# Performance work log

Hardware: AMD Instinct MI355X
Metric: run time of the kernel (lower is better)

The kernel has to match this reference:

```python
import jax, jax.numpy as jnp
import numpy as np

B, L, D, K = 1024, 50, 128, 20
NI, NL, NT = 100000, 10000, 2000  # items, locs, times


def _emb(k, n, d):
    e = jax.random.normal(k, (n, d), dtype=jnp.float32) * 0.02
    return e.at[0].set(0.0)  # padding_idx=0


def setup_inputs() -> dict:
    key = jax.random.key(0)
    ks = jax.random.split(key, 40)
    inp = {}
    inp['item'] = jax.random.randint(ks[0], (B, L), 0, NI)
    inp['locs'] = jax.random.randint(ks[1], (B,), 0, NL)
    inp['times'] = jax.random.randint(ks[2], (B,), 0, NT)
    inp['session_emb'] = jax.random.normal(ks[3], (B, 1, D), dtype=jnp.float32)
    # embedding tables
    inp['loc_emb'] = _emb(ks[4], NL, D)
    inp['time_emb'] = _emb(ks[5], NT, D)
    inp['item_emb'] = _emb(ks[6], NI, D)
    # sampled fixed-fanout neighbor tables Hg[edge]['neighbor']
    inp['nb_IL'] = jax.random.randint(ks[7], (NL, K), 0, NI)   # item neighbors of locs
    inp['nb_TL'] = jax.random.randint(ks[8], (NL, K), 0, NT)   # time neighbors of locs
    inp['nb_IT'] = jax.random.randint(ks[9], (NT, K), 0, NI)   # item neighbors of times
    inp['nb_LT'] = jax.random.randint(ks[10], (NT, K), 0, NL)  # loc neighbors of times
    inp['nb_II'] = jax.random.randint(ks[11], (NI, K), 0, NI)  # item neighbors of items
    inp['nb_LI'] = jax.random.randint(ks[12], (NI, K), 0, NL)  # loc neighbors of items
    inp['nb_TI'] = jax.random.randint(ks[13], (NI, K), 0, NT)  # time neighbors of items
    # 7 HeteAggregator params: Linear(2D -> D) + ReLU
    s = 1.0 / np.sqrt(2 * D)
    names = ['IL', 'TL', 'IT', 'LT', 'II', 'LI', 'TI']
    for i, nm in enumerate(names):
        inp['W_' + nm] = jax.random.uniform(ks[14 + i], (2 * D, D), jnp.float32, -s, s)
        inp['b_' + nm] = jnp.zeros((D,), jnp.float32)
    # 3 SemanticAttention params: Linear(D->D,bias)+tanh, Linear(D->1,no bias)
    s2 = 1.0 / np.sqrt(D)
    for i, nm in enumerate(['l', 't', 'i']):
        inp['Ws_' + nm] = jax.random.uniform(ks[24 + 3 * i], (D, D), jnp.float32, -s2, s2)
        inp['bs_' + nm] = jnp.zeros((D,), jnp.float32)
        inp['q_' + nm] = jax.random.uniform(ks[25 + 3 * i], (D, 1), jnp.float32, -s2, s2)
    return inp


def hete_agg(h_self, h_neigh, W, b):
    # h_self: [N, D]; h_neigh: [N, K, D] -> mean-aggregate, concat, linear, relu
    agg = h_neigh.mean(axis=1)
    return jax.nn.relu(jnp.concatenate([h_self, agg], axis=-1) @ W + b)


def sem_att(z, Ws, bs, q):
    # HAN-style semantic attention. z: [N, M, D]
    w = jnp.tanh(z @ Ws + bs) @ q          # [N, M, 1]
    beta = jax.nn.softmax(w.mean(axis=0), axis=0)  # [M, 1]
    return (beta[None] * z).sum(axis=1)    # [N, D]


def reference(item, locs, times, session_emb,
              loc_emb, time_emb, item_emb,
              nb_IL, nb_TL, nb_IT, nb_LT, nb_II, nb_LI, nb_TI,
              W_IL, b_IL, W_TL, b_TL, W_IT, b_IT, W_LT, b_LT,
              W_II, b_II, W_LI, b_LI, W_TI, b_TI,
              Ws_l, bs_l, q_l, Ws_t, bs_t, q_t, Ws_i, bs_i, q_i):
    iids = item.reshape(-1)  # [B*L]
    h_l_IL = hete_agg(loc_emb[locs], item_emb[nb_IL[locs]], W_IL, b_IL)
    h_l_TL = hete_agg(loc_emb[locs], time_emb[nb_TL[locs]], W_TL, b_TL)
    h_t_IT = hete_agg(time_emb[times], item_emb[nb_IT[times]], W_IT, b_IT)
    h_t_LT = hete_agg(time_emb[times], loc_emb[nb_LT[times]], W_LT, b_LT)
    h_i_II = hete_agg(item_emb[iids], item_emb[nb_II[iids]], W_II, b_II)
    h_i_LI = hete_agg(item_emb[iids], loc_emb[nb_LI[iids]], W_LI, b_LI)
    h_i_TI = hete_agg(item_emb[iids], time_emb[nb_TI[iids]], W_TI, b_TI)
    h_s = session_emb.squeeze(1)  # [B, D]
    h_l_stack = jnp.stack([h_l_IL, h_l_TL, h_s], axis=1)
    h_t_stack = jnp.stack([h_t_IT, h_t_LT, h_s], axis=1)
    h_i_stack = jnp.stack([h_i_II, h_i_TI, h_i_LI], axis=1)
    h_items = sem_att(h_i_stack, Ws_i, bs_i, q_i)
    h_locs = sem_att(h_l_stack, Ws_l, bs_l, q_l)
    h_times = sem_att(h_t_stack, Ws_t, bs_t, q_t)
    return (h_items, h_locs, h_times)
```

## Files before the change

kernel.cpp:

```cpp
#include <hip/hip_runtime.h>
#include <hip/hip_fp16.h>

#define DD 128
#define KK 20
#define TRR 32
#define NT 512

typedef unsigned int uint_t;
typedef unsigned short ushort_t;
typedef unsigned char uchar_t;
typedef _Float16 f16x8 __attribute__((ext_vector_type(8)));
typedef _Float16 f16x2 __attribute__((ext_vector_type(2)));
typedef float f32x4 __attribute__((ext_vector_type(4)));
typedef float f32x2 __attribute__((ext_vector_type(2)));

union UH { __half h; ushort_t s; };
union UF { f16x2 v[4]; uint4 u4; };

#if __has_builtin(__builtin_amdgcn_cvt_scalef32_pk_f16_fp8)
#define HAVE_SCALEF32 1
#endif

__device__ __forceinline__ float fast_tanh(float x) {
  const float e = __expf(2.f * x);
  return 1.f - 2.f / (e + 1.f);
}

__device__ __forceinline__ void f8acc(f16x2* a, const uint2 v) {
#ifdef HAVE_SCALEF32
  a[0] += __builtin_amdgcn_cvt_scalef32_pk_f16_fp8(v.x, 1.0f, false);
  a[1] += __builtin_amdgcn_cvt_scalef32_pk_f16_fp8(v.x, 1.0f, true);
  a[2] += __builtin_amdgcn_cvt_scalef32_pk_f16_fp8(v.y, 1.0f, false);
  a[3] += __builtin_amdgcn_cvt_scalef32_pk_f16_fp8(v.y, 1.0f, true);
#else
  f32x2 p;
  p = __builtin_amdgcn_cvt_pk_f32_fp8(v.x, false);
  a[0] += __builtin_amdgcn_cvt_pkrtz(p[0], p[1]);
  p = __builtin_amdgcn_cvt_pk_f32_fp8(v.x, true);
  a[1] += __builtin_amdgcn_cvt_pkrtz(p[0], p[1]);
  p = __builtin_amdgcn_cvt_pk_f32_fp8(v.y, false);
  a[2] += __builtin_amdgcn_cvt_pkrtz(p[0], p[1]);
  p = __builtin_amdgcn_cvt_pk_f32_fp8(v.y, true);
  a[3] += __builtin_amdgcn_cvt_pkrtz(p[0], p[1]);
#endif
}

struct CvtArgs {
  const float* item; const float* loc; const float* timet;
  ushort_t* dst16; uchar_t* dst8;
};

__global__ __launch_bounds__(256)
void k_cvt3(CvtArgs a) {
  const int t = blockIdx.x * blockDim.x + threadIdx.x;
  const float* src;
  if (t < 1600000) src = a.item + (size_t)t * 8;
  else if (t < 1760000) src = a.loc + ((size_t)t - 1600000) * 8;
  else src = a.timet + ((size_t)t - 1760000) * 8;
  const float4* ip = reinterpret_cast<const float4*>(src);
  const float4 x = ip[0], y = ip[1];
  UH h[8];
  h[0].h = __float2half_rn(x.x); h[1].h = __float2half_rn(x.y);
  h[2].h = __float2half_rn(x.z); h[3].h = __float2half_rn(x.w);
  h[4].h = __float2half_rn(y.x); h[5].h = __float2half_rn(y.y);
  h[6].h = __float2half_rn(y.z); h[7].h = __float2half_rn(y.w);
  uint4 o;
  o.x = (uint_t)h[0].s | ((uint_t)h[1].s << 16);
  o.y = (uint_t)h[2].s | ((uint_t)h[3].s << 16);
  o.z = (uint_t)h[4].s | ((uint_t)h[5].s << 16);
  o.w = (uint_t)h[6].s | ((uint_t)h[7].s << 16);
  reinterpret_cast<uint4*>(a.dst16)[t] = o;
  uint_t p0 = __builtin_amdgcn_cvt_pk_fp8_f32(x.x, x.y, 0u, false);
  p0 = __builtin_amdgcn_cvt_pk_fp8_f32(x.z, x.w, p0, true);
  uint_t p1 = __builtin_amdgcn_cvt_pk_fp8_f32(y.x, y.y, 0u, false);
  p1 = __builtin_amdgcn_cvt_pk_fp8_f32(y.z, y.w, p1, true);
  uint2 q; q.x = p0; q.y = p1;
  reinterpret_cast<uint2*>(a.dst8)[t] = q;
}

struct PackArgs {
  const float* src[10];
  ushort_t* dst;
};

__global__ __launch_bounds__(256)
void k_pack10(PackArgs a) {
  const int b = blockIdx.x, tid = threadIdx.x;
  int job, tin;
  size_t doff;
  if (b < 112) {
    job = b >> 4; tin = ((b & 15) << 8) | tid;
    doff = (size_t)job * 32768;
  } else {
    job = 7 + ((b - 112) >> 3); tin = (((b - 112) & 7) << 8) | tid;
    doff = 7ull * 32768 + (size_t)(job - 7) * 16384;
  }
  const float* W = a.src[job];
  const int l = tin & 63;
  const int ktnt = tin >> 6;
  const int nt = ktnt & 7;
  const int kt = ktnt >> 3;
  const int col = nt * 16 + (l & 15);
  const int kb = kt * 32 + ((l >> 4) << 3);
  UH h[8];
#pragma unroll
  for (int j = 0; j < 8; ++j) h[j].h = __float2half_rn(W[(size_t)(kb + j) * DD + col]);
  uint4 o;
  o.x = (uint_t)h[0].s | ((uint_t)h[1].s << 16);
  o.y = (uint_t)h[2].s | ((uint_t)h[3].s << 16);
  o.z = (uint_t)h[4].s | ((uint_t)h[5].s << 16);
  o.w = (uint_t)h[6].s | ((uint_t)h[7].s << 16);
  *reinterpret_cast<uint4*>(a.dst + doff + (size_t)ktnt * 512 + l * 8) = o;
}

struct MegaArgs {
  const int* item_idx; const ushort_t* item_t;
  const int* nbI[3]; const uchar_t* embI[3]; const ushort_t* pWI[3]; const float* bI[3];
  const ushort_t* pWsI; const float* bsI; const float* qI;
  ushort_t* hI; float* wsumI;
  const int* sidx[2]; const ushort_t* st[2];
  const int* nbS[2][2]; const uchar_t* embS[2][2];
  const ushort_t* pWS[2][2]; const float* bS[2][2];
  const ushort_t* pWsS[2]; const float* bsS[2]; const float* qS[2];
  const float* session;
  ushort_t* hS[2]; float* wsumS[2];
};

__global__ __launch_bounds__(NT, 6)
void k_mega(MegaArgs a) {
  __shared__ int ids[TRR];
  __shared__ int nidx[3][TRR][KK];
  __shared__ __align__(16) ushort_t xs[TRR][4 * DD + 8];
  __shared__ float red[8][TRR];

  const int tid = threadIdx.x;
  const int l = tid & 63;
  const int w = tid >> 6;
  const int bid = blockIdx.x;

  const bool isS = bid < 64;
  const int g = isS ? (bid >> 5) : 0;
  const int bl = isS ? (bid & 31) : (bid - 64);
  const int n0 = bl * TRR;

  const int* sidx;
  const ushort_t* selft;
  const int* nb_[3];
  const uchar_t* emb_[3];
  const ushort_t* pW_[3];
  const float* bias_[3];
  const ushort_t* pws; const float* bss; const float* qp;
  ushort_t* hd; float* wbase;
  if (!isS) {
    sidx = a.item_idx; selft = a.item_t;
    nb_[0] = a.nbI[0]; nb_[1] = a.nbI[1]; nb_[2] = a.nbI[2];
    emb_[0] = a.embI[0]; emb_[1] = a.embI[1]; emb_[2] = a.embI[2];
    pW_[0] = a.pWI[0]; pW_[1] = a.pWI[1]; pW_[2] = a.pWI[2];
    bias_[0] = a.bI[0]; bias_[1] = a.bI[1]; bias_[2] = a.bI[2];
    pws = a.pWsI; bss = a.bsI; qp = a.qI;
    hd = a.hI; wbase = a.wsumI;
  } else if (g == 0) {
    sidx = a.sidx[0]; selft = a.st[0];
    nb_[0] = a.nbS[0][0]; nb_[1] = a.nbS[0][1]; nb_[2] = nullptr;
    emb_[0] = a.embS[0][0]; emb_[1] = a.embS[0][1]; emb_[2] = nullptr;
    pW_[0] = a.pWS[0][0]; pW_[1] = a.pWS[0][1]; pW_[2] = nullptr;
    bias_[0] = a.bS[0][0]; bias_[1] = a.bS[0][1]; bias_[2] = nullptr;
    pws = a.pWsS[0]; bss = a.bsS[0]; qp = a.qS[0];
    hd = a.hS[0]; wbase = a.wsumS[0];
  } else {
    sidx = a.sidx[1]; selft = a.st[1];
    nb_[0] = a.nbS[1][0]; nb_[1] = a.nbS[1][1]; nb_[2] = nullptr;
    emb_[0] = a.embS[1][0]; emb_[1] = a.embS[1][1]; emb_[2] = nullptr;
    pW_[0] = a.pWS[1][0]; pW_[1] = a.pWS[1][1]; pW_[2] = nullptr;
    bias_[0] = a.bS[1][0]; bias_[1] = a.bS[1][1]; bias_[2] = nullptr;
    pws = a.pWsS[1]; bss = a.bsS[1]; qp = a.qS[1];
    hd = a.hS[1]; wbase = a.wsumS[1];
  }

  if (tid < TRR) ids[tid] = sidx[n0 + tid];
  __syncthreads();

  const int gr = tid >> 4;
  const int gsl = tid & 15;

#pragma unroll
  for (int e = 0; e < 3; ++e) {
    if (nb_[e]) {
      for (int t = tid; t < TRR * KK; t += NT) {
        const int rr = t / KK, kk = t - rr * KK;
        nidx[e][rr][kk] = nb_[e][(size_t)ids[rr] * KK + kk];
      }
    }
  }
  *reinterpret_cast<uint4*>(&xs[gr][gsl * 8]) =
      *reinterpret_cast<const uint4*>(selft + ((size_t)ids[gr] << 7) + gsl * 8);
  __syncthreads();

  const _Float16 sch = (_Float16)(1.f / KK);
  const f16x2 scv = (f16x2){sch, sch};
  if (!isS) {
    UF A0, A1, A2;
#pragma unroll
    for (int i = 0; i < 4; ++i) {
      A0.v[i] = (f16x2)0; A1.v[i] = (f16x2)0; A2.v[i] = (f16x2)0;
    }
#pragma unroll
    for (int kb = 0; kb < KK; kb += 4) {
      uint2 u0[4], u1[4], u2[4];
#pragma unroll
      for (int j = 0; j < 4; ++j)
        u0[j] = *reinterpret_cast<const uint2*>(emb_[0] + ((size_t)nidx[0][gr][kb + j] << 7) + gsl * 8);
#pragma unroll
      for (int j = 0; j < 4; ++j)
        u1[j] = *reinterpret_cast<const uint2*>(emb_[1] + ((size_t)nidx[1][gr][kb + j] << 7) + gsl * 8);
#pragma unroll
      for (int j = 0; j < 4; ++j)
        u2[j] = *reinterpret_cast<const uint2*>(emb_[2] + ((size_t)nidx[2][gr][kb + j] << 7) + gsl * 8);
#pragma unroll
      for (int j = 0; j < 4; ++j) {
        f8acc(A0.v, u0[j]); f8acc(A1.v, u1[j]); f8acc(A2.v, u2[j]);
      }
    }
#pragma unroll
    for (int i = 0; i < 4; ++i) {
      A0.v[i] *= scv; A1.v[i] *= scv; A2.v[i] *= scv;
    }
    *reinterpret_cast<uint4*>(&xs[gr][1 * DD + gsl * 8]) = A0.u4;
    *reinterpret_cast<uint4*>(&xs[gr][2 * DD + gsl * 8]) = A1.u4;
    *reinterpret_cast<uint4*>(&xs[gr][3 * DD + gsl * 8]) = A2.u4;
  } else {
    UF A0, A1;
#pragma unroll
    for (int i = 0; i < 4; ++i) { A0.v[i] = (f16x2)0; A1.v[i] = (f16x2)0; }
#pragma unroll
    for (int kb = 0; kb < KK; kb += 5) {
      uint2 u0[5], u1[5];
#pragma unroll
      for (int j = 0; j < 5; ++j)
        u0[j] = *reinterpret_cast<const uint2*>(emb_[0] + ((size_t)nidx[0][gr][kb + j] << 7) + gsl * 8);
#pragma unroll
      for (int j = 0; j < 5; ++j)
        u1[j] = *reinterpret_cast<const uint2*>(emb_[1] + ((size_t)nidx[1][gr][kb + j] << 7) + gsl * 8);
#pragma unroll
      for (int j = 0; j < 5; ++j) { f8acc(A0.v, u0[j]); f8acc(A1.v, u1[j]); }
    }
#pragma unroll
    for (int i = 0; i < 4; ++i) { A0.v[i] *= scv; A1.v[i] *= scv; }
    *reinterpret_cast<uint4*>(&xs[gr][1 * DD + gsl * 8]) = A0.u4;
    *reinterpret_cast<uint4*>(&xs[gr][2 * DD + gsl * 8]) = A1.u4;
    const float* srow = a.session + (size_t)(n0 + gr) * DD + gsl * 8;
    const float4 v0 = *reinterpret_cast<const float4*>(srow);
    const float4 v1 = *reinterpret_cast<const float4*>(srow + 4);
    UH h0, h1, h2, h3, h4, h5, h6, h7;
    h0.h = __float2half_rn(v0.x); h1.h = __float2half_rn(v0.y);
    h2.h = __float2half_rn(v0.z); h3.h = __float2half_rn(v0.w);
    h4.h = __float2half_rn(v1.x); h5.h = __float2half_rn(v1.y);
    h6.h = __float2half_rn(v1.z); h7.h = __float2half_rn(v1.w);
    uint4 o;
    o.x = (uint_t)h0.s | ((uint_t)h1.s << 16);
    o.y = (uint_t)h2.s | ((uint_t)h3.s << 16);
    o.z = (uint_t)h4.s | ((uint_t)h5.s << 16);
    o.w = (uint_t)h6.s | ((uint_t)h7.s << 16);
    *reinterpret_cast<uint4*>(&xs[gr][3 * DD + gsl * 8]) = o;
    *reinterpret_cast<uint4*>(hd + (size_t)(n0 + gr) * 3 * DD + 2 * DD + gsl * 8) = o;
  }
  __syncthreads();

  const int lcol = l & 15;
  const int g8 = (l >> 4) << 3;
  const int col0 = w * 16 + lcol;

#pragma unroll
  for (int e = 0; e < 3; ++e) {
    const bool full = (!isS) || (e < 2);
    if (full) {
      const ushort_t* pWp = pW_[e];
      const float* bp = bias_[e];
      f32x4 acc0, acc1;
      {
        const float b0 = bp[col0];
        acc0 = (f32x4){b0, b0, b0, b0};
        acc1 = acc0;
#pragma unroll
        for (int kt = 0; kt < 8; ++kt) {
          const int xcol = (kt < 4) ? (kt * 32 + g8) : (e * DD + kt * 32 + g8);
          const f16x8 Aa = *reinterpret_cast<const f16x8*>((const void*)&xs[lcol][xcol]);
          const f16x8 Ab = *reinterpret_cast<const f16x8*>((const void*)&xs[16 + lcol][xcol]);
          const f16x8 B = *reinterpret_cast<const f16x8*>(
              (const void*)(pWp + ((size_t)(kt * 8 + w) * 512) + l * 8));
          acc0 = __builtin_amdgcn_mfma_f32_16x16x32_f16(Aa, B, acc0, 0, 0, 0);
          acc1 = __builtin_amdgcn_mfma_f32_16x16x32_f16(Ab, B, acc1, 0, 0, 0);
        }
#pragma unroll
        for (int j = 0; j < 4; ++j) {
          acc0[j] = fmaxf(acc0[j], 0.f);
          acc1[j] = fmaxf(acc1[j], 0.f);
        }
      }
      __syncthreads();
      {
        const int rbase = (l >> 4) << 2;
#pragma unroll
        for (int j = 0; j < 4; ++j) {
          const int r0 = rbase + j, r1 = 16 + rbase + j;
          UH h0, h1;
          h0.h = __float2half_rn(acc0[j]);
          h1.h = __float2half_rn(acc1[j]);
          hd[(size_t)(n0 + r0) * 3 * DD + e * DD + col0] = h0.s;
          hd[(size_t)(n0 + r1) * 3 * DD + e * DD + col0] = h1.s;
          xs[r0][(e + 1) * DD + col0] = h0.s;
          xs[r1][(e + 1) * DD + col0] = h1.s;
        }
      }
      __syncthreads();
    }
    {
      const float b0 = bss[col0];
      f32x4 s0 = (f32x4){b0, b0, b0, b0};
      f32x4 s1 = s0;
#pragma unroll
      for (int kt = 0; kt < 4; ++kt) {
        const f16x8 Aa = *reinterpret_cast<const f16x8*>(
            (const void*)&xs[lcol][(e + 1) * DD + kt * 32 + g8]);
        const f16x8 Ab = *reinterpret_cast<const f16x8*>(
            (const void*)&xs[16 + lcol][(e + 1) * DD + kt * 32 + g8]);
        const f16x8 B = *reinterpret_cast<const f16x8*>(
            (const void*)(pws + ((size_t)(kt * 8 + w) * 512) + l * 8));
        s0 = __builtin_amdgcn_mfma_f32_16x16x32_f16(Aa, B, s0, 0, 0, 0);
        s1 = __builtin_amdgcn_mfma_f32_16x16x32_f16(Ab, B, s1, 0, 0, 0);
      }
      const float q0 = qp[col0];
      float p0[4], p1[4];
#pragma unroll
      for (int j = 0; j < 4; ++j) {
        p0[j] = fast_tanh(s0[j]) * q0;
        p1[j] = fast_tanh(s1[j]) * q0;
      }
#pragma unroll
      for (int off = 1; off < 16; off <<= 1) {
#pragma unroll
        for (int j = 0; j < 4; ++j) {
          p0[j] += __shfl_xor(p0[j], off, 64);
          p1[j] += __shfl_xor(p1[j], off, 64);
        }
      }
      if (lcol == 0) {
        const int rbase = (l >> 4) << 2;
#pragma unroll
        for (int j = 0; j < 4; ++j) {
          red[w][rbase + j] = p0[j];
          red[w][16 + rbase + j] = p1[j];
        }
      }
    }
    __syncthreads();
    if (tid < TRR) {
      float s = 0.f;
#pragma unroll
      for (int ww = 0; ww < 8; ++ww) s += red[ww][tid];
#pragma unroll
      for (int off = 1; off < 32; off <<= 1) s += __shfl_xor(s, off, 64);
      if (tid == 0) atomicAdd(&wbase[(bl & 63) * 4 + e], s);
    }
    __syncthreads();
  }
}

__global__ void k_beta(const float* __restrict__ wsum, float* __restrict__ beta) {
  if (threadIdx.x == 0 && blockIdx.x == 0) {
    const float invN[3] = {1.f / 51200.f, 1.f / 1024.f, 1.f / 1024.f};
    for (int g = 0; g < 3; ++g) {
      float s0 = 0.f, s1 = 0.f, s2 = 0.f;
      for (int bkt = 0; bkt < 64; ++bkt) {
        s0 += wsum[g * 256 + bkt * 4 + 0];
        s1 += wsum[g * 256 + bkt * 4 + 1];
        s2 += wsum[g * 256 + bkt * 4 + 2];
      }
      s0 *= invN[g]; s1 *= invN[g]; s2 *= invN[g];
      const float mx = fmaxf(s0, fmaxf(s1, s2));
      const float e0 = expf(s0 - mx), e1 = expf(s1 - mx), e2 = expf(s2 - mx);
      const float inv = 1.f / (e0 + e1 + e2);
      beta[g * 4 + 0] = e0 * inv;
      beta[g * 4 + 1] = e1 * inv;
      beta[g * 4 + 2] = e2 * inv;
    }
  }
}

__global__ void k_out(const ushort_t* __restrict__ h, const float* __restrict__ beta,
                      float* __restrict__ out) {
  const int idx = blockIdx.x * blockDim.x + threadIdx.x;
  const int row = idx >> 7;
  const int g = (row < 51200) ? 0 : ((row < 52224) ? 1 : 2);
  const float* bt = beta + g * 4;
  const size_t base = (size_t)idx + (size_t)row * 2 * DD;
  UH a, b, c;
  a.s = h[base]; b.s = h[base + DD]; c.s = h[base + 2 * DD];
  out[idx] = bt[0] * __half2float(a.h) + bt[1] * __half2float(b.h) +
             bt[2] * __half2float(c.h);
}


extern "C" void kernel_launch(void* const* d_in, const int* in_sizes, int n_in,
                              void* d_out, int out_size, void* d_ws, size_t ws_size,
                              hipStream_t stream) {
  const int*   item     = (const int*)  d_in[0];
  const int*   locs     = (const int*)  d_in[1];
  const int*   times    = (const int*)  d_in[2];
  const float* session  = (const float*)d_in[3];
  const float* loc_emb  = (const float*)d_in[4];
  const float* time_emb = (const float*)d_in[5];
  const float* item_emb = (const float*)d_in[6];
  const int* nb_IL = (const int*)d_in[7];
  const int* nb_TL = (const int*)d_in[8];
  const int* nb_IT = (const int*)d_in[9];
  const int* nb_LT = (const int*)d_in[10];
  const int* nb_II = (const int*)d_in[11];
  const int* nb_LI = (const int*)d_in[12];
  const int* nb_TI = (const int*)d_in[13];
  const float* W_IL = (const float*)d_in[14]; const float* b_IL = (const float*)d_in[15];
  const float* W_TL = (const float*)d_in[16]; const float* b_TL = (const float*)d_in[17];
  const float* W_IT = (const float*)d_in[18]; const float* b_IT = (const float*)d_in[19];
  const float* W_LT = (const float*)d_in[20]; const float* b_LT = (const float*)d_in[21];
  const float* W_II = (const float*)d_in[22]; const float* b_II = (const float*)d_in[23];
  const float* W_LI = (const float*)d_in[24]; const float* b_LI = (const float*)d_in[25];
  const float* W_TI = (const float*)d_in[26]; const float* b_TI = (const float*)d_in[27];
  const float* Ws_l = (const float*)d_in[28]; const float* bs_l = (const float*)d_in[29];
  const float* q_l  = (const float*)d_in[30];
  const float* Ws_t = (const float*)d_in[31]; const float* bs_t = (const float*)d_in[32];
  const float* q_t  = (const float*)d_in[33];
  const float* Ws_i = (const float*)d_in[34]; const float* bs_i = (const float*)d_in[35];
  const float* q_i  = (const float*)d_in[36];

  float* outp = (float*)d_out;

  char* wsb = (char*)d_ws;
  float* wsum  = (float*)wsb;
  float* betap = (float*)wsb + 1024;
  ushort_t* pk = (ushort_t*)(wsb + 16384);
  ushort_t* pk_II = pk;
  ushort_t* pk_TI = pk_II + 32768;
  ushort_t* pk_LI = pk_TI + 32768;
  ushort_t* pk_IL = pk_LI + 32768;
  ushort_t* pk_TL = pk_IL + 32768;
  ushort_t* pk_IT = pk_TL + 32768;
  ushort_t* pk_LT = pk_IT + 32768;
  ushort_t* pk_Wi = pk_LT + 32768;
  ushort_t* pk_Wl = pk_Wi + 16384;
  ushort_t* pk_Wt = pk_Wl + 16384;
  ushort_t* hbuf  = pk_Wt + 16384;
  ushort_t* item_h = hbuf + (size_t)53248 * 3 * DD;
  ushort_t* loc_h  = item_h + (size_t)100000 * DD;
  ushort_t* time_h = loc_h + (size_t)10000 * DD;
  uchar_t* item_8 = (uchar_t*)(time_h + (size_t)2000 * DD);
  uchar_t* loc_8  = item_8 + (size_t)100000 * DD;
  uchar_t* time_8 = loc_8 + (size_t)10000 * DD;

  hipMemsetAsync(d_ws, 0, 16384, stream);

  CvtArgs ca;
  ca.item = item_emb; ca.loc = loc_emb; ca.timet = time_emb;
  ca.dst16 = item_h; ca.dst8 = item_8;
  k_cvt3<<<dim3(7000), dim3(256), 0, stream>>>(ca);

  PackArgs pa;
  pa.src[0] = W_II; pa.src[1] = W_TI; pa.src[2] = W_LI;
  pa.src[3] = W_IL; pa.src[4] = W_TL; pa.src[5] = W_IT; pa.src[6] = W_LT;
  pa.src[7] = Ws_i; pa.src[8] = Ws_l; pa.src[9] = Ws_t;
  pa.dst = pk;
  k_pack10<<<dim3(136), dim3(256), 0, stream>>>(pa);

  ushort_t* h_items = hbuf;
  ushort_t* h_locs  = hbuf + (size_t)51200 * 3 * DD;
  ushort_t* h_times = hbuf + (size_t)52224 * 3 * DD;

  MegaArgs ma;
  ma.item_idx = item; ma.item_t = item_h;
  ma.nbI[0] = nb_II; ma.nbI[1] = nb_TI; ma.nbI[2] = nb_LI;
  ma.embI[0] = item_8; ma.embI[1] = time_8; ma.embI[2] = loc_8;
  ma.pWI[0] = pk_II; ma.pWI[1] = pk_TI; ma.pWI[2] = pk_LI;
  ma.bI[0] = b_II; ma.bI[1] = b_TI; ma.bI[2] = b_LI;
  ma.pWsI = pk_Wi; ma.bsI = bs_i; ma.qI = q_i;
  ma.hI = h_items; ma.wsumI = wsum + 0;
  ma.sidx[0] = locs;  ma.sidx[1] = times;
  ma.st[0] = loc_h;   ma.st[1] = time_h;
  ma.nbS[0][0] = nb_IL; ma.nbS[0][1] = nb_TL;
  ma.nbS[1][0] = nb_IT; ma.nbS[1][1] = nb_LT;
  ma.embS[0][0] = item_8; ma.embS[0][1] = time_8;
  ma.embS[1][0] = item_8; ma.embS[1][1] = loc_8;
  ma.pWS[0][0] = pk_IL; ma.pWS[0][1] = pk_TL;
  ma.pWS[1][0] = pk_IT; ma.pWS[1][1] = pk_LT;
  ma.bS[0][0] = b_IL; ma.bS[0][1] = b_TL;
  ma.bS[1][0] = b_IT; ma.bS[1][1] = b_LT;
  ma.pWsS[0] = pk_Wl; ma.pWsS[1] = pk_Wt;
  ma.bsS[0] = bs_l; ma.bsS[1] = bs_t;
  ma.qS[0] = q_l; ma.qS[1] = q_t;
  ma.session = session;
  ma.hS[0] = h_locs; ma.hS[1] = h_times;
  ma.wsumS[0] = wsum + 256; ma.wsumS[1] = wsum + 512;
  k_mega<<<dim3(64 + 51200 / TRR), dim3(NT), 0, stream>>>(ma);

  k_beta<<<dim3(1), dim3(64), 0, stream>>>(wsum, betap);
  k_out<<<dim3((53248 * 128) / 256), dim3(256), 0, stream>>>(hbuf, betap, outp);
}
```

Before: 123.0 us.

## Pipeline neighbor gathers with MFMA stages and drop fp16 table conversion

The fp16 copy of the embedding tables is no longer written. Self embeddings are now read from the fp8 tables and converted in-kernel, which removes a large write stream from the conversion kernel. In the item path, the gather for the next edge type is issued into registers before the current edge's MFMA and attention stages, so memory latency overlaps compute. It also uses lightweight LDS-only barriers and lowers the occupancy hint, trading higher register pressure for overlap, and self embeddings now carry fp8 precision.

After: 191.7 us. 1.56x slower.

```diff
diff --git a/kernel.cpp b/kernel.cpp
--- a/kernel.cpp
+++ b/kernel.cpp
@@ -11,11 +11,13 @@
 typedef unsigned char uchar_t;
 typedef _Float16 f16x8 __attribute__((ext_vector_type(8)));
 typedef _Float16 f16x2 __attribute__((ext_vector_type(2)));
+typedef __fp16 h16x2 __attribute__((ext_vector_type(2)));
 typedef float f32x4 __attribute__((ext_vector_type(4)));
 typedef float f32x2 __attribute__((ext_vector_type(2)));
 
 union UH { __half h; ushort_t s; };
 union UF { f16x2 v[4]; uint4 u4; };
+union CV { h16x2 a; f16x2 b; };
 
 #if __has_builtin(__builtin_amdgcn_cvt_scalef32_pk_f16_fp8)
 #define HAVE_SCALEF32 1
@@ -26,28 +28,42 @@
   return 1.f - 2.f / (e + 1.f);
 }
 
-__device__ __forceinline__ void f8acc(f16x2* a, const uint2 v) {
+__device__ __forceinline__ void lgkm_bar() {
+  asm volatile("s_waitcnt lgkmcnt(0)" ::: "memory");
+  __builtin_amdgcn_s_barrier();
+  __builtin_amdgcn_sched_barrier(0);
+}
+
+__device__ __forceinline__ UF f8cvt(const uint2 v) {
+  UF r;
 #ifdef HAVE_SCALEF32
-  a[0] += __builtin_amdgcn_cvt_scalef32_pk_f16_fp8(v.x, 1.0f, false);
-  a[1] += __builtin_amdgcn_cvt_scalef32_pk_f16_fp8(v.x, 1.0f, true);
-  a[2] += __builtin_amdgcn_cvt_scalef32_pk_f16_fp8(v.y, 1.0f, false);
-  a[3] += __builtin_amdgcn_cvt_scalef32_pk_f16_fp8(v.y, 1.0f, true);
+  r.v[0] = __builtin_amdgcn_cvt_scalef32_pk_f16_fp8(v.x, 1.0f, false);
+  r.v[1] = __builtin_amdgcn_cvt_scalef32_pk_f16_fp8(v.x, 1.0f, true);
+  r.v[2] = __builtin_amdgcn_cvt_scalef32_pk_f16_fp8(v.y, 1.0f, false);
+  r.v[3] = __builtin_amdgcn_cvt_scalef32_pk_f16_fp8(v.y, 1.0f, true);
 #else
   f32x2 p;
+  CV c;
   p = __builtin_amdgcn_cvt_pk_f32_fp8(v.x, false);
-  a[0] += __builtin_amdgcn_cvt_pkrtz(p[0], p[1]);
+  c.a = __builtin_amdgcn_cvt_pkrtz(p[0], p[1]); r.v[0] = c.b;
   p = __builtin_amdgcn_cvt_pk_f32_fp8(v.x, true);
-  a[1] += __builtin_amdgcn_cvt_pkrtz(p[0], p[1]);
+  c.a = __builtin_amdgcn_cvt_pkrtz(p[0], p[1]); r.v[1] = c.b;
   p = __builtin_amdgcn_cvt_pk_f32_fp8(v.y, false);
-  a[2] += __builtin_amdgcn_cvt_pkrtz(p[0], p[1]);
+  c.a = __builtin_amdgcn_cvt_pkrtz(p[0], p[1]); r.v[2] = c.b;
   p = __builtin_amdgcn_cvt_pk_f32_fp8(v.y, true);
-  a[3] += __builtin_amdgcn_cvt_pkrtz(p[0], p[1]);
+  c.a = __builtin_amdgcn_cvt_pkrtz(p[0], p[1]); r.v[3] = c.b;
 #endif
+  return r;
+}
+
+__device__ __forceinline__ void f8acc(f16x2* a, const uint2 v) {
+  const UF r = f8cvt(v);
+  a[0] += r.v[0]; a[1] += r.v[1]; a[2] += r.v[2]; a[3] += r.v[3];
 }
 
 struct CvtArgs {
   const float* item; const float* loc; const float* timet;
-  ushort_t* dst16; uchar_t* dst8;
+  uchar_t* dst8;
 };
 
 __global__ __launch_bounds__(256)
@@ -59,17 +75,6 @@
   else src = a.timet + ((size_t)t - 1760000) * 8;
   const float4* ip = reinterpret_cast<const float4*>(src);
   const float4 x = ip[0], y = ip[1];
-  UH h[8];
-  h[0].h = __float2half_rn(x.x); h[1].h = __float2half_rn(x.y);
-  h[2].h = __float2half_rn(x.z); h[3].h = __float2half_rn(x.w);
-  h[4].h = __float2half_rn(y.x); h[5].h = __float2half_rn(y.y);
-  h[6].h = __float2half_rn(y.z); h[7].h = __float2half_rn(y.w);
-  uint4 o;
-  o.x = (uint_t)h[0].s | ((uint_t)h[1].s << 16);
-  o.y = (uint_t)h[2].s | ((uint_t)h[3].s << 16);
-  o.z = (uint_t)h[4].s | ((uint_t)h[5].s << 16);
-  o.w = (uint_t)h[6].s | ((uint_t)h[7].s << 16);
-  reinterpret_cast<uint4*>(a.dst16)[t] = o;
   uint_t p0 = __builtin_amdgcn_cvt_pk_fp8_f32(x.x, x.y, 0u, false);
   p0 = __builtin_amdgcn_cvt_pk_fp8_f32(x.z, x.w, p0, true);
   uint_t p1 = __builtin_amdgcn_cvt_pk_fp8_f32(y.x, y.y, 0u, false);
@@ -114,11 +119,11 @@
 }
 
 struct MegaArgs {
-  const int* item_idx; const ushort_t* item_t;
+  const int* item_idx;
   const int* nbI[3]; const uchar_t* embI[3]; const ushort_t* pWI[3]; const float* bI[3];
   const ushort_t* pWsI; const float* bsI; const float* qI;
   ushort_t* hI; float* wsumI;
-  const int* sidx[2]; const ushort_t* st[2];
+  const int* sidx[2]; const uchar_t* st[2];
   const int* nbS[2][2]; const uchar_t* embS[2][2];
   const ushort_t* pWS[2][2]; const float* bS[2][2];
   const ushort_t* pWsS[2]; const float* bsS[2]; const float* qS[2];
@@ -126,7 +131,7 @@
   ushort_t* hS[2]; float* wsumS[2];
 };
 
-__global__ __launch_bounds__(NT, 6)
+__global__ __launch_bounds__(NT, 5)
 void k_mega(MegaArgs a) {
   __shared__ int ids[TRR];
   __shared__ int nidx[3][TRR][KK];
@@ -144,7 +149,7 @@
   const int n0 = bl * TRR;
 
   const int* sidx;
-  const ushort_t* selft;
+  const uchar_t* self8;
   const int* nb_[3];
   const uchar_t* emb_[3];
   const ushort_t* pW_[3];
@@ -152,7 +157,7 @@
   const ushort_t* pws; const float* bss; const float* qp;
   ushort_t* hd; float* wbase;
   if (!isS) {
-    sidx = a.item_idx; selft = a.item_t;
+    sidx = a.item_idx; self8 = a.embI[0];
     nb_[0] = a.nbI[0]; nb_[1] = a.nbI[1]; nb_[2] = a.nbI[2];
     emb_[0] = a.embI[0]; emb_[1] = a.embI[1]; emb_[2] = a.embI[2];
     pW_[0] = a.pWI[0]; pW_[1] = a.pWI[1]; pW_[2] = a.pWI[2];
@@ -160,7 +165,7 @@
     pws = a.pWsI; bss = a.bsI; qp = a.qI;
     hd = a.hI; wbase = a.wsumI;
   } else if (g == 0) {
-    sidx = a.sidx[0]; selft = a.st[0];
+    sidx = a.sidx[0]; self8 = a.st[0];
     nb_[0] = a.nbS[0][0]; nb_[1] = a.nbS[0][1]; nb_[2] = nullptr;
     emb_[0] = a.embS[0][0]; emb_[1] = a.embS[0][1]; emb_[2] = nullptr;
     pW_[0] = a.pWS[0][0]; pW_[1] = a.pWS[0][1]; pW_[2] = nullptr;
@@ -168,7 +173,7 @@
     pws = a.pWsS[0]; bss = a.bsS[0]; qp = a.qS[0];
     hd = a.hS[0]; wbase = a.wsumS[0];
   } else {
-    sidx = a.sidx[1]; selft = a.st[1];
+    sidx = a.sidx[1]; self8 = a.st[1];
     nb_[0] = a.nbS[1][0]; nb_[1] = a.nbS[1][1]; nb_[2] = nullptr;
     emb_[0] = a.embS[1][0]; emb_[1] = a.embS[1][1]; emb_[2] = nullptr;
     pW_[0] = a.pWS[1][0]; pW_[1] = a.pWS[1][1]; pW_[2] = nullptr;
@@ -192,93 +197,51 @@
       }
     }
   }
-  *reinterpret_cast<uint4*>(&xs[gr][gsl * 8]) =
-      *reinterpret_cast<const uint4*>(selft + ((size_t)ids[gr] << 7) + gsl * 8);
+  {
+    const uint2 su = *reinterpret_cast<const uint2*>(
+        self8 + ((size_t)ids[gr] << 7) + gsl * 8);
+    const UF S0 = f8cvt(su);
+    *reinterpret_cast<uint4*>(&xs[gr][gsl * 8]) = S0.u4;
+  }
   __syncthreads();
 
   const _Float16 sch = (_Float16)(1.f / KK);
   const f16x2 scv = (f16x2){sch, sch};
-  if (!isS) {
-    UF A0, A1, A2;
-#pragma unroll
-    for (int i = 0; i < 4; ++i) {
-      A0.v[i] = (f16x2)0; A1.v[i] = (f16x2)0; A2.v[i] = (f16x2)0;
-    }
-#pragma unroll
-    for (int kb = 0; kb < KK; kb += 4) {
-      uint2 u0[4], u1[4], u2[4];
-#pragma unroll
-      for (int j = 0; j < 4; ++j)
-        u0[j] = *reinterpret_cast<const uint2*>(emb_[0] + ((size_t)nidx[0][gr][kb + j] << 7) + gsl * 8);
-#pragma unroll
-      for (int j = 0; j < 4; ++j)
-        u1[j] = *reinterpret_cast<const uint2*>(emb_[1] + ((size_t)nidx[1][gr][kb + j] << 7) + gsl * 8);
-#pragma unroll
-      for (int j = 0; j < 4; ++j)
-        u2[j] = *reinterpret_cast<const uint2*>(emb_[2] + ((size_t)nidx[2][gr][kb + j] << 7) + gsl * 8);
-#pragma unroll
-      for (int j = 0; j < 4; ++j) {
-        f8acc(A0.v, u0[j]); f8acc(A1.v, u1[j]); f8acc(A2.v, u2[j]);
-      }
-    }
-#pragma unroll
-    for (int i = 0; i < 4; ++i) {
-      A0.v[i] *= scv; A1.v[i] *= scv; A2.v[i] *= scv;
-    }
-    *reinterpret_cast<uint4*>(&xs[gr][1 * DD + gsl * 8]) = A0.u4;
-    *reinterpret_cast<uint4*>(&xs[gr][2 * DD + gsl * 8]) = A1.u4;
-    *reinterpret_cast<uint4*>(&xs[gr][3 * DD + gsl * 8]) = A2.u4;
-  } else {
-    UF A0, A1;
-#pragma unroll
-    for (int i = 0; i < 4; ++i) { A0.v[i] = (f16x2)0; A1.v[i] = (f16x2)0; }
-#pragma unroll
-    for (int kb = 0; kb < KK; kb += 5) {
-      uint2 u0[5], u1[5];
-#pragma unroll
-      for (int j = 0; j < 5; ++j)
-        u0[j] = *reinterpret_cast<const uint2*>(emb_[0] + ((size_t)nidx[0][gr][kb + j] << 7) + gsl * 8);
-#pragma unroll
-      for (int j = 0; j < 5; ++j)
-        u1[j] = *reinterpret_cast<const uint2*>(emb_[1] + ((size_t)nidx[1][gr][kb + j] << 7) + gsl * 8);
-#pragma unroll
-      for (int j = 0; j < 5; ++j) { f8acc(A0.v, u0[j]); f8acc(A1.v, u1[j]); }
-    }
-#pragma unroll
-    for (int i = 0; i < 4; ++i) { A0.v[i] *= scv; A1.v[i] *= scv; }
-    *reinterpret_cast<uint4*>(&xs[gr][1 * DD + gsl * 8]) = A0.u4;
-    *reinterpret_cast<uint4*>(&xs[gr][2 * DD + gsl * 8]) = A1.u4;
-    const float* srow = a.session + (size_t)(n0 + gr) * DD + gsl * 8;
-    const float4 v0 = *reinterpret_cast<const float4*>(srow);
-    const float4 v1 = *reinterpret_cast<const float4*>(srow + 4);
-    UH h0, h1, h2, h3, h4, h5, h6, h7;
-    h0.h = __float2half_rn(v0.x); h1.h = __float2half_rn(v0.y);
-    h2.h = __float2half_rn(v0.z); h3.h = __float2half_rn(v0.w);
-    h4.h = __float2half_rn(v1.x); h5.h = __float2half_rn(v1.y);
-    h6.h = __float2half_rn(v1.z); h7.h = __float2half_rn(v1.w);
-    uint4 o;
-    o.x = (uint_t)h0.s | ((uint_t)h1.s << 16);
-    o.y = (uint_t)h2.s | ((uint_t)h3.s << 16);
-    o.z = (uint_t)h4.s | ((uint_t)h5.s << 16);
-    o.w = (uint_t)h6.s | ((uint_t)h7.s << 16);
-    *reinterpret_cast<uint4*>(&xs[gr][3 * DD + gsl * 8]) = o;
-    *reinterpret_cast<uint4*>(hd + (size_t)(n0 + gr) * 3 * DD + 2 * DD + gsl * 8) = o;
-  }
-  __syncthreads();
-
   const int lcol = l & 15;
   const int g8 = (l >> 4) << 3;
   const int col0 = w * 16 + lcol;
 
-#pragma unroll
-  for (int e = 0; e < 3; ++e) {
-    const bool full = (!isS) || (e < 2);
-    if (full) {
-      const ushort_t* pWp = pW_[e];
-      const float* bp = bias_[e];
+  if (!isS) {
+    {
+      UF A;
+#pragma unroll
+      for (int i = 0; i < 4; ++i) A.v[i] = (f16x2)0;
+      uint2 u[KK];
+#pragma unroll
+      for (int k = 0; k < KK; ++k)
+        u[k] = *reinterpret_cast<const uint2*>(
+            emb_[0] + ((size_t)nidx[0][gr][k] << 7) + gsl * 8);
+#pragma unroll
+      for (int k = 0; k < KK; ++k) f8acc(A.v, u[k]);
+#pragma unroll
+      for (int i = 0; i < 4; ++i) A.v[i] *= scv;
+      *reinterpret_cast<uint4*>(&xs[gr][1 * DD + gsl * 8]) = A.u4;
+    }
+    lgkm_bar();
+
+    uint2 hold[KK];
+#pragma unroll
+    for (int e = 0; e < 3; ++e) {
+      if (e < 2) {
+#pragma unroll
+        for (int k = 0; k < KK; ++k)
+          hold[k] = *reinterpret_cast<const uint2*>(
+              emb_[e + 1] + ((size_t)nidx[e + 1][gr][k] << 7) + gsl * 8);
+        __builtin_amdgcn_sched_barrier(0);
+      }
       f32x4 acc0, acc1;
       {
-        const float b0 = bp[col0];
+        const float b0 = bias_[e][col0];
         acc0 = (f32x4){b0, b0, b0, b0};
         acc1 = acc0;
 #pragma unroll
@@ -287,7 +250,7 @@
           const f16x8 Aa = *reinterpret_cast<const f16x8*>((const void*)&xs[lcol][xcol]);
           const f16x8 Ab = *reinterpret_cast<const f16x8*>((const void*)&xs[16 + lcol][xcol]);
           const f16x8 B = *reinterpret_cast<const f16x8*>(
-              (const void*)(pWp + ((size_t)(kt * 8 + w) * 512) + l * 8));
+              (const void*)(pW_[e] + ((size_t)(kt * 8 + w) * 512) + l * 8));
           acc0 = __builtin_amdgcn_mfma_f32_16x16x32_f16(Aa, B, acc0, 0, 0, 0);
           acc1 = __builtin_amdgcn_mfma_f32_16x16x32_f16(Ab, B, acc1, 0, 0, 0);
         }
@@ -297,7 +260,7 @@
           acc1[j] = fmaxf(acc1[j], 0.f);
         }
       }
-      __syncthreads();
+      lgkm_bar();
       {
         const int rbase = (l >> 4) << 2;
 #pragma unroll
@@ -312,57 +275,200 @@
           xs[r1][(e + 1) * DD + col0] = h1.s;
         }
       }
+      lgkm_bar();
+      {
+        const float b0 = bss[col0];
+        f32x4 s0 = (f32x4){b0, b0, b0, b0};
+        f32x4 s1 = s0;
+#pragma unroll
+        for (int kt = 0; kt < 4; ++kt) {
+          const f16x8 Aa = *reinterpret_cast<const f16x8*>(
+              (const void*)&xs[lcol][(e + 1) * DD + kt * 32 + g8]);
+          const f16x8 Ab = *reinterpret_cast<const f16x8*>(
+              (const void*)&xs[16 + lcol][(e + 1) * DD + kt * 32 + g8]);
+          const f16x8 B = *reinterpret_cast<const f16x8*>(
+              (const void*)(pws + ((size_t)(kt * 8 + w) * 512) + l * 8));
+          s0 = __builtin_amdgcn_mfma_f32_16x16x32_f16(Aa, B, s0, 0, 0, 0);
+          s1 = __builtin_amdgcn_mfma_f32_16x16x32_f16(Ab, B, s1, 0, 0, 0);
+        }
+        const float q0 = qp[col0];
+        float p0[4], p1[4];
+#pragma unroll
+        for (int j = 0; j < 4; ++j) {
+          p0[j] = fast_tanh(s0[j]) * q0;
+          p1[j] = fast_tanh(s1[j]) * q0;
+        }
+#pragma unroll
+        for (int off = 1; off < 16; off <<= 1) {
+#pragma unroll
+          for (int j = 0; j < 4; ++j) {
+            p0[j] += __shfl_xor(p0[j], off, 64);
+            p1[j] += __shfl_xor(p1[j], off, 64);
+          }
+        }
+        if (lcol == 0) {
+          const int rbase = (l >> 4) << 2;
+#pragma unroll
+          for (int j = 0; j < 4; ++j) {
+            red[w][rbase + j] = p0[j];
+            red[w][16 + rbase + j] = p1[j];
+          }
+        }
+      }
+      lgkm_bar();
+      if (tid < TRR) {
+        float s = 0.f;
+#pragma unroll
+        for (int ww = 0; ww < 8; ++ww) s += red[ww][tid];
+#pragma unroll
+        for (int off = 1; off < 32; off <<= 1) s += __shfl_xor(s, off, 64);
+        if (tid == 0) atomicAdd(&wbase[(bl & 63) * 4 + e], s);
+      }
+      if (e < 2) {
+        UF A;
+#pragma unroll
+        for (int i = 0; i < 4; ++i) A.v[i] = (f16x2)0;
+#pragma unroll
+        for (int k = 0; k < KK; ++k) f8acc(A.v, hold[k]);
+#pragma unroll
+        for (int i = 0; i < 4; ++i) A.v[i] *= scv;
+        *reinterpret_cast<uint4*>(&xs[gr][(e + 2) * DD + gsl * 8]) = A.u4;
+      }
+      lgkm_bar();
+    }
+  } else {
+    {
+      UF A0, A1;
+#pragma unroll
+      for (int i = 0; i < 4; ++i) { A0.v[i] = (f16x2)0; A1.v[i] = (f16x2)0; }
+#pragma unroll
+      for (int kb = 0; kb < KK; kb += 5) {
+        uint2 u0[5], u1[5];
+#pragma unroll
+        for (int j = 0; j < 5; ++j)
+          u0[j] = *reinterpret_cast<const uint2*>(
+              emb_[0] + ((size_t)nidx[0][gr][kb + j] << 7) + gsl * 8);
+#pragma unroll
+        for (int j = 0; j < 5; ++j)
+          u1[j] = *reinterpret_cast<const uint2*>(
+              emb_[1] + ((size_t)nidx[1][gr][kb + j] << 7) + gsl * 8);
+#pragma unroll
+        for (int j = 0; j < 5; ++j) { f8acc(A0.v, u0[j]); f8acc(A1.v, u1[j]); }
+      }
+#pragma unroll
+      for (int i = 0; i < 4; ++i) { A0.v[i] *= scv; A1.v[i] *= scv; }
+      *reinterpret_cast<uint4*>(&xs[gr][1 * DD + gsl * 8]) = A0.u4;
+      *reinterpret_cast<uint4*>(&xs[gr][2 * DD + gsl * 8]) = A1.u4;
+      const float* srow = a.session + (size_t)(n0 + gr) * DD + gsl * 8;
+      const float4 v0 = *reinterpret_cast<const float4*>(srow);
+      const float4 v1 = *reinterpret_cast<const float4*>(srow + 4);
+      UH h0, h1, h2, h3, h4, h5, h6, h7;
+      h0.h = __float2half_rn(v0.x); h1.h = __float2half_rn(v0.y);
+      h2.h = __float2half_rn(v0.z); h3.h = __float2half_rn(v0.w);
+      h4.h = __float2half_rn(v1.x); h5.h = __float2half_rn(v1.y);
+      h6.h = __float2half_rn(v1.z); h7.h = __float2half_rn(v1.w);
+      uint4 o;
+      o.x = (uint_t)h0.s | ((uint_t)h1.s << 16);
+      o.y = (uint_t)h2.s | ((uint_t)h3.s << 16);
+      o.z = (uint_t)h4.s | ((uint_t)h5.s << 16);
+      o.w = (uint_t)h6.s | ((uint_t)h7.s << 16);
+      *reinterpret_cast<uint4*>(&xs[gr][3 * DD + gsl * 8]) = o;
+      *reinterpret_cast<uint4*>(hd + (size_t)(n0 + gr) * 3 * DD + 2 * DD + gsl * 8) = o;
+    }
+    __syncthreads();
+
+#pragma unroll
+    for (int e = 0; e < 3; ++e) {
+      const bool full = (e < 2);
+      if (full) {
+        f32x4 acc0, acc1;
+        {
+          const float b0 = bias_[e][col0];
+          acc0 = (f32x4){b0, b0, b0, b0};
+          acc1 = acc0;
+#pragma unroll
+          for (int kt = 0; kt < 8; ++kt) {
+            const int xcol = (kt < 4) ? (kt * 32 + g8) : (e * DD + kt * 32 + g8);
+            const f16x8 Aa = *reinterpret_cast<const f16x8*>((const void*)&xs[lcol][xcol]);
+            const f16x8 Ab = *reinterpret_cast<const f16x8*>((const void*)&xs[16 + lcol][xcol]);
+            const f16x8 B = *reinterpret_cast<const f16x8*>(
+                (const void*)(pW_[e] + ((size_t)(kt * 8 + w) * 512) + l * 8));
+            acc0 = __builtin_amdgcn_mfma_f32_16x16x32_f16(Aa, B, acc0, 0, 0, 0);
+            acc1 = __builtin_amdgcn_mfma_f32_16x16x32_f16(Ab, B, acc1, 0, 0, 0);
+          }
+#pragma unroll
+          for (int j = 0; j < 4; ++j) {
+            acc0[j] = fmaxf(acc0[j], 0.f);
+            acc1[j] = fmaxf(acc1[j], 0.f);
+          }
+        }
+        __syncthreads();
+        {
+          const int rbase = (l >> 4) << 2;
+#pragma unroll
+          for (int j = 0; j < 4; ++j) {
+            const int r0 = rbase + j, r1 = 16 + rbase + j;
+            UH h0, h1;
+            h0.h = __float2half_rn(acc0[j]);
+            h1.h = __float2half_rn(acc1[j]);
+            hd[(size_t)(n0 + r0) * 3 * DD + e * DD + col0] = h0.s;
+            hd[(size_t)(n0 + r1) * 3 * DD + e * DD + col0] = h1.s;
+            xs[r0][(e + 1) * DD + col0] = h0.s;
+            xs[r1][(e + 1) * DD + col0] = h1.s;
+          }
+        }
+        __syncthreads();
+      }
+      {
+        const float b0 = bss[col0];
+        f32x4 s0 = (f32x4){b0, b0, b0, b0};
+        f32x4 s1 = s0;
+#pragma unroll
+        for (int kt = 0; kt < 4; ++kt) {
+          const f16x8 Aa = *reinterpret_cast<const f16x8*>(
+              (const void*)&xs[lcol][(e + 1) * DD + kt * 32 + g8]);
+          const f16x8 Ab = *reinterpret_cast<const f16x8*>(
+              (const void*)&xs[16 + lcol][(e + 1) * DD + kt * 32 + g8]);
+          const f16x8 B = *reinterpret_cast<const f16x8*>(
+              (const void*)(pws + ((size_t)(kt * 8 + w) * 512) + l * 8));
+          s0 = __builtin_amdgcn_mfma_f32_16x16x32_f16(Aa, B, s0, 0, 0, 0);
+          s1 = __builtin_amdgcn_mfma_f32_16x16x32_f16(Ab, B, s1, 0, 0, 0);
+        }
+        const float q0 = qp[col0];
+        float p0[4], p1[4];
+#pragma unroll
+        for (int j = 0; j < 4; ++j) {
+          p0[j] = fast_tanh(s0[j]) * q0;
+          p1[j] = fast_tanh(s1[j]) * q0;
+        }
+#pragma unroll
+        for (int off = 1; off < 16; off <<= 1) {
+#pragma unroll
+          for (int j = 0; j < 4; ++j) {
+            p0[j] += __shfl_xor(p0[j], off, 64);
+            p1[j] += __shfl_xor(p1[j], off, 64);
+          }
+        }
+        if (lcol == 0) {
+          const int rbase = (l >> 4) << 2;
+#pragma unroll
+          for (int j = 0; j < 4; ++j) {
+            red[w][rbase + j] = p0[j];
+            red[w][16 + rbase + j] = p1[j];
+          }
+        }
+      }
+      __syncthreads();
+      if (tid < TRR) {
+        float s = 0.f;
+#pragma unroll
+        for (int ww = 0; ww < 8; ++ww) s += red[ww][tid];
+#pragma unroll
+        for (int off = 1; off < 32; off <<= 1) s += __shfl_xor(s, off, 64);
+        if (tid == 0) atomicAdd(&wbase[(bl & 63) * 4 + e], s);
+      }
       __syncthreads();
     }
-    {
-      const float b0 = bss[col0];
-      f32x4 s0 = (f32x4){b0, b0, b0, b0};
-      f32x4 s1 = s0;
-#pragma unroll
-      for (int kt = 0; kt < 4; ++kt) {
-        const f16x8 Aa = *reinterpret_cast<const f16x8*>(
-            (const void*)&xs[lcol][(e + 1) * DD + kt * 32 + g8]);
-        const f16x8 Ab = *reinterpret_cast<const f16x8*>(
-            (const void*)&xs[16 + lcol][(e + 1) * DD + kt * 32 + g8]);
-        const f16x8 B = *reinterpret_cast<const f16x8*>(
-            (const void*)(pws + ((size_t)(kt * 8 + w) * 512) + l * 8));
-        s0 = __builtin_amdgcn_mfma_f32_16x16x32_f16(Aa, B, s0, 0, 0, 0);
-        s1 = __builtin_amdgcn_mfma_f32_16x16x32_f16(Ab, B, s1, 0, 0, 0);
-      }
-      const float q0 = qp[col0];
-      float p0[4], p1[4];
-#pragma unroll
-      for (int j = 0; j < 4; ++j) {
-        p0[j] = fast_tanh(s0[j]) * q0;
-        p1[j] = fast_tanh(s1[j]) * q0;
-      }
-#pragma unroll
-      for (int off = 1; off < 16; off <<= 1) {
-#pragma unroll
-        for (int j = 0; j < 4; ++j) {
-          p0[j] += __shfl_xor(p0[j], off, 64);
-          p1[j] += __shfl_xor(p1[j], off, 64);
-        }
-      }
-      if (lcol == 0) {
-        const int rbase = (l >> 4) << 2;
-#pragma unroll
-        for (int j = 0; j < 4; ++j) {
-          red[w][rbase + j] = p0[j];
-          red[w][16 + rbase + j] = p1[j];
-        }
-      }
-    }
-    __syncthreads();
-    if (tid < TRR) {
-      float s = 0.f;
-#pragma unroll
-      for (int ww = 0; ww < 8; ++ww) s += red[ww][tid];
-#pragma unroll
-      for (int off = 1; off < 32; off <<= 1) s += __shfl_xor(s, off, 64);
-      if (tid == 0) atomicAdd(&wbase[(bl & 63) * 4 + e], s);
-    }
-    __syncthreads();
   }
 }
 
@@ -449,18 +555,15 @@
   ushort_t* pk_Wl = pk_Wi + 16384;
   ushort_t* pk_Wt = pk_Wl + 16384;
   ushort_t* hbuf  = pk_Wt + 16384;
-  ushort_t* item_h = hbuf + (size_t)53248 * 3 * DD;
-  ushort_t* loc_h  = item_h + (size_t)100000 * DD;
-  ushort_t* time_h = loc_h + (size_t)10000 * DD;
-  uchar_t* item_8 = (uchar_t*)(time_h + (size_t)2000 * DD);
+  uchar_t* item_8 = (uchar_t*)(hbuf + (size_t)53248 * 3 * DD);
   uchar_t* loc_8  = item_8 + (size_t)100000 * DD;
   uchar_t* time_8 = loc_8 + (size_t)10000 * DD;
 
-  hipMemsetAsync(d_ws, 0, 16384, stream);
+  (void)hipMemsetAsync(d_ws, 0, 16384, stream);
 
   CvtArgs ca;
   ca.item = item_emb; ca.loc = loc_emb; ca.timet = time_emb;
-  ca.dst16 = item_h; ca.dst8 = item_8;
+  ca.dst8 = item_8;
   k_cvt3<<<dim3(7000), dim3(256), 0, stream>>>(ca);
 
   PackArgs pa;
@@ -475,7 +578,7 @@
   ushort_t* h_times = hbuf + (size_t)52224 * 3 * DD;
 
   MegaArgs ma;
-  ma.item_idx = item; ma.item_t = item_h;
+  ma.item_idx = item;
   ma.nbI[0] = nb_II; ma.nbI[1] = nb_TI; ma.nbI[2] = nb_LI;
   ma.embI[0] = item_8; ma.embI[1] = time_8; ma.embI[2] = loc_8;
   ma.pWI[0] = pk_II; ma.pWI[1] = pk_TI; ma.pWI[2] = pk_LI;
@@ -483,7 +586,7 @@
   ma.pWsI = pk_Wi; ma.bsI = bs_i; ma.qI = q_i;
   ma.hI = h_items; ma.wsumI = wsum + 0;
   ma.sidx[0] = locs;  ma.sidx[1] = times;
-  ma.st[0] = loc_h;   ma.st[1] = time_h;
+  ma.st[0] = loc_8;   ma.st[1] = time_8;
   ma.nbS[0][0] = nb_IL; ma.nbS[0][1] = nb_TL;
   ma.nbS[1][0] = nb_IT; ma.nbS[1][1] = nb_LT;
   ma.embS[0][0] = item_8; ma.embS[0][1] = time_8;
```
